# Performance work log

Measured on AMD Instinct MI355X. Metric: run time of the kernel, lower is better.

The kernel has to match this reference:

```python
import jax, jax.numpy as jnp
import numpy as np

B = 16          # graphs per batch
NPER = 1024     # nodes per graph (max_nodes for to_dense_batch)
N = B * NPER    # total nodes
D = 128         # hidden_dim
H = 8           # nhead
E = 524288      # total edges (avg degree 32)
DFF = 512       # dim_feedforward
LN_EPS = 1e-5


def setup_inputs() -> dict:
    key = jax.random.key(0)
    ks = jax.random.split(key, 26)
    w = lambda k, shape, s=0.05: (jax.random.normal(k, shape, jnp.float32) * s)
    h = jax.random.normal(ks[0], (N, D), jnp.float32)
    edge_index = jax.random.randint(ks[1], (2, E), 0, N, jnp.int32)
    edge_attr = jax.random.normal(ks[2], (E, D), jnp.float32)
    # nodes are in a random 'original' order; sort_idx sorts them by graph id
    sort_idx = jax.random.permutation(ks[3], N).astype(jnp.int32)
    unsort_idx = jnp.argsort(sort_idx).astype(jnp.int32)
    sorted_batch = jnp.repeat(jnp.arange(B, dtype=jnp.int32), NPER)
    batch = jnp.zeros((N,), jnp.int32).at[sort_idx].set(sorted_batch)
    return {
        "h": h, "edge_attr": edge_attr,
        # GINEConv: edge linear + 2-layer gin MLP
        "edge_w": w(ks[4], (D, D)), "edge_b": w(ks[5], (D,)),
        "gin_w1": w(ks[6], (D, D)), "gin_b1": w(ks[7], (D,)),
        "gin_w2": w(ks[8], (D, D)), "gin_b2": w(ks[9], (D,)),
        # MultiheadAttention packed qkv + out proj
        "in_proj_w": w(ks[10], (3 * D, D)), "in_proj_b": w(ks[11], (3 * D,)),
        "out_w": w(ks[12], (D, D)), "out_b": w(ks[13], (D,)),
        # FFN
        "ffn_w1": w(ks[14], (DFF, D)), "ffn_b1": w(ks[15], (DFF,)),
        "ffn_w2": w(ks[16], (D, DFF)), "ffn_b2": w(ks[17], (D,)),
        # LayerNorms
        "ln1_w": jnp.ones((D,)), "ln1_b": jnp.zeros((D,)),
        "ln2_w": jnp.ones((D,)), "ln2_b": jnp.zeros((D,)),
        "ln3_w": jnp.ones((D,)), "ln3_b": jnp.zeros((D,)),
        "edge_index": edge_index, "batch": batch,
        "sort_idx": sort_idx, "unsort_idx": unsort_idx,
    }


def _layer_norm(x, w, b):
    mu = x.mean(-1, keepdims=True)
    var = ((x - mu) ** 2).mean(-1, keepdims=True)
    return (x - mu) * jax.lax.rsqrt(var + LN_EPS) * w + b


def reference(h, edge_attr, edge_w, edge_b, gin_w1, gin_b1, gin_w2, gin_b2,
              in_proj_w, in_proj_b, out_w, out_b,
              ffn_w1, ffn_b1, ffn_w2, ffn_b2,
              ln1_w, ln1_b, ln2_w, ln2_b, ln3_w, ln3_b,
              edge_index, batch, sort_idx, unsort_idx):
    residual = h
    # ---- local branch: GINEConv (eps=0) -----------------------------------
    src, dst = edge_index[0], edge_index[1]
    e = edge_attr @ edge_w.T + edge_b                      # [E, D]
    msg = jax.nn.relu(h[src] + e)                          # gather + fuse
    agg = jax.ops.segment_sum(msg, dst, num_segments=N)    # scatter-add
    x = h + agg                                            # (1+eps)*x_i + aggr
    h_local = jax.nn.relu(x @ gin_w1.T + gin_b1) @ gin_w2.T + gin_b2
    # ---- global branch: sort -> dense batch -> MHA -> unsort --------------
    hs = h[sort_idx]
    bs = batch[sort_idx]
    counts = jax.ops.segment_sum(jnp.ones((N,), jnp.int32), bs, num_segments=B)
    ptr = jnp.concatenate([jnp.zeros((1,), jnp.int32),
                           jnp.cumsum(counts)[:-1].astype(jnp.int32)])
    pos = jnp.arange(N, dtype=jnp.int32) - ptr[bs]         # slot within graph
    dense = jnp.zeros((B, NPER, D), h.dtype).at[bs, pos].set(hs)
    mask = jnp.zeros((B, NPER), bool).at[bs, pos].set(True)
    qkv = dense @ in_proj_w.T + in_proj_b                  # [B, NPER, 3D]
    q, k, v = jnp.split(qkv, 3, axis=-1)
    hd = D // H
    q = q.reshape(B, NPER, H, hd)
    k = k.reshape(B, NPER, H, hd)
    v = v.reshape(B, NPER, H, hd)
    scores = jnp.einsum('bqhd,bkhd->bhqk', q, k) / np.float32(np.sqrt(hd))
    scores = jnp.where(mask[:, None, None, :], scores, jnp.float32(-1e9))
    attn = jax.nn.softmax(scores, axis=-1)
    ao = jnp.einsum('bhqk,bkhd->bqhd', attn, v).reshape(B, NPER, D)
    ao = ao @ out_w.T + out_b
    h_attn = ao[bs, pos][unsort_idx]                       # dense->flat->unsort
    # ---- residual + norms + FFN -------------------------------------------
    h1 = _layer_norm(residual + h_local, ln1_w, ln1_b)
    h2 = _layer_norm(h1 + h_attn, ln2_w, ln2_b)
    ffn = jax.nn.gelu(h2 @ ffn_w1.T + ffn_b1, approximate=False) @ ffn_w2.T + ffn_b2
    return _layer_norm(h2 + ffn, ln3_w, ln3_b)
```

## Files before the change

kernel.cpp:

```cpp
#include <hip/hip_runtime.h>
#include <cmath>

typedef __attribute__((ext_vector_type(4))) float  f32x4;
typedef __attribute__((ext_vector_type(16))) float f32x16;
typedef __attribute__((ext_vector_type(2))) float  f32x2;
typedef __attribute__((ext_vector_type(8))) short  s16x8;
typedef __attribute__((ext_vector_type(4))) short  s16x4;
typedef __attribute__((ext_vector_type(2))) short  s16x2;
typedef __attribute__((ext_vector_type(4))) int    i32x4;

#define DEV __device__ __forceinline__

DEV float bf2f(short s) {
    unsigned int u = ((unsigned int)(unsigned short)s) << 16;
    return __builtin_bit_cast(float, u);
}
DEV short f2bs(float f) {
    unsigned int x = __builtin_bit_cast(unsigned int, f);
    x += 0x7fffu + ((x >> 16) & 1u);
    return (short)(x >> 16);
}
DEV s16x8 ld8(const void* p, size_t off, int m) {
    s16x8 r;
    if (m) {
        const float* f = (const float*)p + off;
        f32x4 a = *(const f32x4*)f, b = *(const f32x4*)(f + 4);
#pragma unroll
        for (int j = 0; j < 4; ++j) { r[j] = f2bs(a[j]); r[4 + j] = f2bs(b[j]); }
    } else {
        r = *(const s16x8*)((const short*)p + off);
    }
    return r;
}
DEV float ldf(const void* p, size_t off, int m) {
    return m ? ((const float*)p)[off] : bf2f(((const short*)p)[off]);
}

__global__ void probe_kernel(const unsigned* __restrict__ w1, int* __restrict__ flag)
{
    if (threadIdx.x == 0 && blockIdx.x == 0)
        flag[0] = (w1[0] == 0x3F800000u) ? 1 : 0;
}

__global__ __launch_bounds__(256, 2)
void edge_kernel(const void* __restrict__ EA, const void* __restrict__ EW,
                 const void* __restrict__ EB, const void* __restrict__ H,
                 const int* __restrict__ esrc, const int* __restrict__ edst,
                 float* __restrict__ agg, const int* __restrict__ modep)
{
    const int m = *modep;
    __shared__ short Ws[128][136];
    int tid = threadIdx.x;
#pragma unroll
    for (int i = 0; i < 8; ++i) {
        int id = i * 256 + tid;
        int r = id >> 4, c = (id & 15) << 3;
        *(s16x8*)&Ws[r][c] = ld8(EW, (size_t)r * 128 + c, m);
    }
    __syncthreads();

    int wave = tid >> 6, lane = tid & 63;
    int lq = lane & 15, quad = lane >> 4;
    int eb = blockIdx.x * 64 + wave * 16;

    s16x8 af[4];
    const size_t abase = (size_t)(eb + lq) * 128 + quad * 8;
#pragma unroll
    for (int kb = 0; kb < 4; ++kb)
        af[kb] = ld8(EA, abase + kb * 32, m);

    i32x4 sv = *(const i32x4*)&esrc[eb + quad * 4];
    i32x4 dv = *(const i32x4*)&edst[eb + quad * 4];

    f32x4 acc[8] = {};
#pragma unroll
    for (int kb = 0; kb < 4; ++kb) {
#pragma unroll
        for (int nt = 0; nt < 8; ++nt) {
            s16x8 bfr = *(const s16x8*)&Ws[nt * 16 + lq][kb * 32 + quad * 8];
            acc[nt] = __builtin_amdgcn_mfma_f32_16x16x32_bf16(af[kb], bfr, acc[nt], 0, 0, 0);
        }
    }
#pragma unroll
    for (int nt = 0; nt < 8; ++nt) {
        int col = nt * 16 + lq;
        float bias = ldf(EB, col, m);
#pragma unroll
        for (int r = 0; r < 4; ++r) {
            float v = acc[nt][r] + bias + ldf(H, (size_t)sv[r] * 128 + col, m);
            v = fmaxf(v, 0.f);
            atomicAdd(&agg[(size_t)dv[r] * 128 + col], v);
        }
    }
}

__global__ void xadd_kernel(const void* __restrict__ H, const float* __restrict__ agg,
                            short* __restrict__ X, const int* __restrict__ modep)
{
    const int m = *modep;
    int i = (blockIdx.x * 256 + threadIdx.x) * 4;
    float hv[4];
    if (m) { f32x4 t = *(const f32x4*)((const float*)H + i);
#pragma unroll
             for (int j = 0; j < 4; ++j) hv[j] = t[j]; }
    else   { s16x4 t = *(const s16x4*)((const short*)H + i);
#pragma unroll
             for (int j = 0; j < 4; ++j) hv[j] = bf2f(t[j]); }
    f32x4 av = *(const f32x4*)&agg[i];
    s16x4 o;
#pragma unroll
    for (int j = 0; j < 4; ++j) o[j] = f2bs(hv[j] + av[j]);
    *(s16x4*)&X[i] = o;
}

template<int KTOT, int ACT, bool GATHER, bool XIN>
__global__ __launch_bounds__(256, 2)
void gemm_bt(const void* __restrict__ X, const int* __restrict__ ridx,
             const void* __restrict__ W, const void* __restrict__ B,
             short* __restrict__ Y, int N, const int* __restrict__ modep)
{
    const int m = *modep;
    const int xm = XIN ? m : 0;
    __shared__ short As[64][136];
    __shared__ short Wsh[64][136];
    int tid = threadIdx.x;
    int wave = tid >> 6, lane = tid & 63;
    int lq = lane & 15, quad = lane >> 4;
    int mbase = blockIdx.x * 64, nbase = blockIdx.y * 64;

    f32x4 acc[4] = {};
    for (int kc = 0; kc < KTOT / 128; ++kc) {
#pragma unroll
        for (int i = 0; i < 4; ++i) {
            int id = i * 256 + tid;
            int r = id >> 4, c = (id & 15) << 3;
            int srow = GATHER ? ridx[mbase + r] : (mbase + r);
            *(s16x8*)&As[r][c]  = ld8(X, (size_t)srow * KTOT + kc * 128 + c, xm);
            *(s16x8*)&Wsh[r][c] = ld8(W, (size_t)(nbase + r) * KTOT + kc * 128 + c, m);
        }
        __syncthreads();
        s16x8 af[4];
#pragma unroll
        for (int kb = 0; kb < 4; ++kb)
            af[kb] = *(const s16x8*)&As[wave * 16 + lq][kb * 32 + quad * 8];
#pragma unroll
        for (int kb = 0; kb < 4; ++kb) {
#pragma unroll
            for (int nt = 0; nt < 4; ++nt) {
                s16x8 bfr = *(const s16x8*)&Wsh[nt * 16 + lq][kb * 32 + quad * 8];
                acc[nt] = __builtin_amdgcn_mfma_f32_16x16x32_bf16(af[kb], bfr, acc[nt], 0, 0, 0);
            }
        }
        __syncthreads();
    }
#pragma unroll
    for (int nt = 0; nt < 4; ++nt) {
        int col = nbase + nt * 16 + lq;
        float bias = ldf(B, col, m);
#pragma unroll
        for (int r = 0; r < 4; ++r) {
            int row = mbase + wave * 16 + quad * 4 + r;
            float v = acc[nt][r] + bias;
            if (ACT == 1) v = fmaxf(v, 0.f);
            if (ACT == 2) v = 0.5f * v * (1.f + erff(v * 0.70710678118f));
            Y[(size_t)row * N + col] = f2bs(v);
        }
    }
}

__global__ __launch_bounds__(256, 2)
void attn_kernel(const short* __restrict__ QKV, short* __restrict__ AO)
{
    __shared__ __align__(16) short Ks[2048][8];
    __shared__ __align__(16) short Vt[16][1032];
    int bid = blockIdx.x;
    int qc = bid & 3, bh = bid >> 2;
    int b = bh >> 3, hh = bh & 7;
    int t = threadIdx.x;
    const short* base = QKV + (size_t)b * 1024 * 384 + hh * 16;

#pragma unroll
    for (int i = 0; i < 8; ++i) {
        int idx = i * 256 + t;
        int c = idx >> 10, kv = idx & 1023;
        const short* r = base + (size_t)kv * 384;
        *(s16x8*)&Ks[c * 1024 + kv][0] = *(const s16x8*)&r[128 + c * 8];
        s16x8 v = *(const s16x8*)&r[256 + c * 8];
#pragma unroll
        for (int j = 0; j < 8; ++j) Vt[c * 8 + j][kv] = v[j];
    }
    __syncthreads();

    int wave = t >> 6, lane = t & 63;
    int ln = lane & 31, hi = lane >> 5;

    for (int t2 = 0; t2 < 2; ++t2) {
        int qrow = qc * 256 + t2 * 128 + wave * 32 + ln;
        s16x8 qf = *(const s16x8*)(base + (size_t)qrow * 384 + hi * 8);
        f32x16 oacc = {};
        f32x16 zacc = {};
        float den = 0.f;
        for (int kv0 = 0; kv0 < 1024; kv0 += 32) {
            s16x8 kf = *(const s16x8*)&Ks[hi * 1024 + kv0 + ln][0];
            f32x16 st = __builtin_amdgcn_mfma_f32_32x32x16_bf16(kf, qf, zacc, 0, 0, 0);
            float e[16];
#pragma unroll
            for (int r2 = 0; r2 < 16; ++r2) {
                e[r2] = __expf(fminf(st[r2] * 0.25f, 30.f));
                den += e[r2];
            }
            unsigned pw[8];
#pragma unroll
            for (int r2 = 0; r2 < 8; ++r2)
                pw[r2] = (unsigned)(unsigned short)f2bs(e[2 * r2])
                       | ((unsigned)(unsigned short)f2bs(e[2 * r2 + 1]) << 16);
            auto sA = __builtin_amdgcn_permlane32_swap((int)pw[0], (int)pw[2], false, false);
            auto sB = __builtin_amdgcn_permlane32_swap((int)pw[1], (int)pw[3], false, false);
            auto sC = __builtin_amdgcn_permlane32_swap((int)pw[4], (int)pw[6], false, false);
            auto sD = __builtin_amdgcn_permlane32_swap((int)pw[5], (int)pw[7], false, false);
            i32x4 f1 = { (int)sA[0], (int)sB[0], (int)sA[1], (int)sB[1] };
            i32x4 f2 = { (int)sC[0], (int)sD[0], (int)sC[1], (int)sD[1] };
            s16x8 vf1 = *(const s16x8*)&Vt[ln & 15][kv0 + hi * 8];
            s16x8 vf2 = *(const s16x8*)&Vt[ln & 15][kv0 + 16 + hi * 8];
            oacc = __builtin_amdgcn_mfma_f32_32x32x16_bf16(vf1, __builtin_bit_cast(s16x8, f1), oacc, 0, 0, 0);
            oacc = __builtin_amdgcn_mfma_f32_32x32x16_bf16(vf2, __builtin_bit_cast(s16x8, f2), oacc, 0, 0, 0);
        }
        den += __shfl_xor(den, 32);
        float inv = 1.f / den;
        short* orow = AO + (size_t)(b * 1024 + qrow) * 128 + hh * 16;
        s16x4 oA, oB;
#pragma unroll
        for (int r2 = 0; r2 < 4; ++r2) {
            oA[r2] = f2bs(oacc[r2] * inv);
            oB[r2] = f2bs(oacc[4 + r2] * inv);
        }
        *(s16x4*)&orow[hi * 4]     = oA;
        *(s16x4*)&orow[8 + hi * 4] = oB;
    }
}

template<bool AIN, bool FINAL>
__global__ __launch_bounds__(256)
void ln_kernel(const void* __restrict__ A, const short* __restrict__ Badd,
               const int* __restrict__ gidx,
               const void* __restrict__ w, const void* __restrict__ bb,
               void* __restrict__ outp, const int* __restrict__ modep)
{
    const int m = *modep;
    int wave = threadIdx.x >> 6, lane = threadIdx.x & 63;
    int row = blockIdx.x * 4 + wave;
    int grow = gidx ? gidx[row] : row;
    int c = lane * 2;
    float a0, a1;
    if (AIN && m) {
        f32x2 t = *(const f32x2*)&((const float*)A)[(size_t)row * 128 + c];
        a0 = t[0]; a1 = t[1];
    } else {
        s16x2 t = *(const s16x2*)&((const short*)A)[(size_t)row * 128 + c];
        a0 = bf2f(t[0]); a1 = bf2f(t[1]);
    }
    s16x2 bv = *(const s16x2*)&Badd[(size_t)grow * 128 + c];
    float x0 = a0 + bf2f(bv[0]);
    float x1 = a1 + bf2f(bv[1]);
    float s = x0 + x1;
#pragma unroll
    for (int o = 1; o < 64; o <<= 1) s += __shfl_xor(s, o);
    float mu = s * (1.f / 128.f);
    float d0 = x0 - mu, d1 = x1 - mu;
    float q = d0 * d0 + d1 * d1;
#pragma unroll
    for (int o = 1; o < 64; o <<= 1) q += __shfl_xor(q, o);
    float rs = rsqrtf(q * (1.f / 128.f) + 1e-5f);
    float y0 = d0 * rs * ldf(w, c, m)     + ldf(bb, c, m);
    float y1 = d1 * rs * ldf(w, c + 1, m) + ldf(bb, c + 1, m);
    if (FINAL && m) {
        f32x2 ov = {y0, y1};
        *(f32x2*)&((float*)outp)[(size_t)row * 128 + c] = ov;
    } else {
        s16x2 ov = {f2bs(y0), f2bs(y1)};
        *(s16x2*)&((short*)outp)[(size_t)row * 128 + c] = ov;
    }
}

extern "C" void kernel_launch(void* const* d_in, const int* in_sizes, int n_in,
                              void* d_out, int out_size, void* d_ws, size_t ws_size,
                              hipStream_t stream)
{
    const void* h   = d_in[0];
    const void* ea  = d_in[1];
    const void* edw = d_in[2];
    const void* edb = d_in[3];
    const void* gw1 = d_in[4];
    const void* gb1 = d_in[5];
    const void* gw2 = d_in[6];
    const void* gb2 = d_in[7];
    const void* ipw = d_in[8];
    const void* ipb = d_in[9];
    const void* ow  = d_in[10];
    const void* ob  = d_in[11];
    const void* fw1 = d_in[12];
    const void* fb1 = d_in[13];
    const void* fw2 = d_in[14];
    const void* fb2 = d_in[15];
    const void* l1w = d_in[16];
    const void* l1b = d_in[17];
    const void* l2w = d_in[18];
    const void* l2b = d_in[19];
    const void* l3w = d_in[20];
    const void* l3b = d_in[21];
    const int* ei    = (const int*)d_in[22];
    const int* sidx  = (const int*)d_in[24];
    const int* uidx  = (const int*)d_in[25];

    const int NN = 16384, EE = 524288;
    const size_t MB = 1024 * 1024;
    char* ws = (char*)d_ws;
    float* agg   = (float*)ws;
    short* mid   = (short*)(ws + 8 * MB);
    short* h1    = (short*)(ws + 12 * MB);
    short* qkv   = (short*)ws;
    short* atns  = (short*)(ws + 16 * MB);
    short* ffmid = (short*)ws;
    short* ffout = (short*)(ws + 16 * MB);
    short* h2    = (short*)(ws + 20 * MB);
    int*   flag  = (int*)(ws + 24 * MB);
    short* xbuf  = (short*)d_out;
    short* hloc  = (short*)d_out;
    short* ao    = (short*)d_out;

    probe_kernel<<<1, 64, 0, stream>>>((const unsigned*)l1w, flag);
    hipMemsetAsync(agg, 0, (size_t)NN * 128 * sizeof(float), stream);
    edge_kernel<<<EE / 64, 256, 0, stream>>>(ea, edw, edb, h, ei, ei + EE, agg, flag);
    xadd_kernel<<<NN * 128 / 1024, 256, 0, stream>>>(h, agg, xbuf, flag);
    gemm_bt<128, 1, false, false><<<dim3(NN / 64, 2), 256, 0, stream>>>(xbuf, nullptr, gw1, gb1, mid, 128, flag);
    gemm_bt<128, 0, false, false><<<dim3(NN / 64, 2), 256, 0, stream>>>(mid, nullptr, gw2, gb2, hloc, 128, flag);
    ln_kernel<true, false><<<NN / 4, 256, 0, stream>>>(h, hloc, nullptr, l1w, l1b, h1, flag);
    gemm_bt<128, 0, true, true><<<dim3(NN / 64, 6), 256, 0, stream>>>(h, sidx, ipw, ipb, qkv, 384, flag);
    attn_kernel<<<512, 256, 0, stream>>>(qkv, ao);
    gemm_bt<128, 0, false, false><<<dim3(NN / 64, 2), 256, 0, stream>>>(ao, nullptr, ow, ob, atns, 128, flag);
    ln_kernel<false, false><<<NN / 4, 256, 0, stream>>>(h1, atns, uidx, l2w, l2b, h2, flag);
    gemm_bt<128, 2, false, false><<<dim3(NN / 64, 8), 256, 0, stream>>>(h2, nullptr, fw1, fb1, ffmid, 512, flag);
    gemm_bt<512, 0, false, false><<<dim3(NN / 64, 2), 256, 0, stream>>>(ffmid, nullptr, fw2, fb2, ffout, 128, flag);
    ln_kernel<false, true><<<NN / 4, 256, 0, stream>>>(h2, ffout, nullptr, l3w, l3b, d_out, flag);
}
```

Measured before the change: 757.2 us.

## Sort edges by destination and aggregate runs before atomic adds

Adds a histogram, a single-block scan and a scatter pass that build a CSR-style ordering of edges by destination node. The edge kernel then walks the sorted edges and sums consecutive same-destination contributions in registers before issuing atomics, which cuts the number of global float atomics. The cost is three extra kernels plus one more memset, gathered rather than contiguous reads of edge_attr through sEid, and run-length merging that only spans 16 edges per lane group, which is about half a node's average degree of 32.

```diff
diff --git a/kernel.cpp b/kernel.cpp
--- a/kernel.cpp
+++ b/kernel.cpp
@@ -42,11 +42,52 @@
         flag[0] = (w1[0] == 0x3F800000u) ? 1 : 0;
 }
 
+__global__ void hist_kernel(const int* __restrict__ edst, int* __restrict__ cnt)
+{
+    int e = blockIdx.x * 256 + threadIdx.x;
+    atomicAdd(&cnt[edst[e]], 1);
+}
+
+__global__ __launch_bounds__(1024)
+void scan_kernel(const int* __restrict__ cnt, int* __restrict__ cursor)
+{
+    __shared__ int s[1024];
+    int t = threadIdx.x;
+    int v[16];
+    int sum = 0;
+#pragma unroll
+    for (int j = 0; j < 16; ++j) { v[j] = cnt[t * 16 + j]; sum += v[j]; }
+    s[t] = sum;
+    __syncthreads();
+    for (int off = 1; off < 1024; off <<= 1) {
+        int x = (t >= off) ? s[t - off] : 0;
+        __syncthreads();
+        s[t] += x;
+        __syncthreads();
+    }
+    int running = s[t] - sum;
+#pragma unroll
+    for (int j = 0; j < 16; ++j) { cursor[t * 16 + j] = running; running += v[j]; }
+}
+
+__global__ void scatter_kernel(const int* __restrict__ esrc, const int* __restrict__ edst,
+                               int* __restrict__ cursor, int* __restrict__ sEid,
+                               int* __restrict__ sDst, int* __restrict__ sSrc)
+{
+    int e = blockIdx.x * 256 + threadIdx.x;
+    int d = edst[e];
+    int pos = atomicAdd(&cursor[d], 1);
+    sEid[pos] = e;
+    sDst[pos] = d;
+    sSrc[pos] = esrc[e];
+}
+
 __global__ __launch_bounds__(256, 2)
-void edge_kernel(const void* __restrict__ EA, const void* __restrict__ EW,
-                 const void* __restrict__ EB, const void* __restrict__ H,
-                 const int* __restrict__ esrc, const int* __restrict__ edst,
-                 float* __restrict__ agg, const int* __restrict__ modep)
+void edge_agg_kernel(const void* __restrict__ EA, const void* __restrict__ EW,
+                     const void* __restrict__ EB, const void* __restrict__ H,
+                     const int* __restrict__ sEid, const int* __restrict__ sDst,
+                     const int* __restrict__ sSrc,
+                     float* __restrict__ agg, const int* __restrict__ modep)
 {
     const int m = *modep;
     __shared__ short Ws[128][136];
@@ -61,36 +102,61 @@
 
     int wave = tid >> 6, lane = tid & 63;
     int lq = lane & 15, quad = lane >> 4;
-    int eb = blockIdx.x * 64 + wave * 16;
-
-    s16x8 af[4];
-    const size_t abase = (size_t)(eb + lq) * 128 + quad * 8;
-#pragma unroll
-    for (int kb = 0; kb < 4; ++kb)
-        af[kb] = ld8(EA, abase + kb * 32, m);
-
-    i32x4 sv = *(const i32x4*)&esrc[eb + quad * 4];
-    i32x4 dv = *(const i32x4*)&edst[eb + quad * 4];
-
-    f32x4 acc[8] = {};
-#pragma unroll
-    for (int kb = 0; kb < 4; ++kb) {
-#pragma unroll
-        for (int nt = 0; nt < 8; ++nt) {
-            s16x8 bfr = *(const s16x8*)&Ws[nt * 16 + lq][kb * 32 + quad * 8];
-            acc[nt] = __builtin_amdgcn_mfma_f32_16x16x32_bf16(af[kb], bfr, acc[nt], 0, 0, 0);
-        }
-    }
-#pragma unroll
-    for (int nt = 0; nt < 8; ++nt) {
-        int col = nt * 16 + lq;
-        float bias = ldf(EB, col, m);
+    int ebw = blockIdx.x * 256 + wave * 64;
+
+    float ebias[8];
+#pragma unroll
+    for (int nt = 0; nt < 8; ++nt) ebias[nt] = ldf(EB, nt * 16 + lq, m);
+
+    float run[8] = {};
+    int run_d = -1;
+
+    for (int t = 0; t < 4; ++t) {
+        int arow = ebw + ((lq >> 2) << 4) + t * 4 + (lq & 3);
+        int aeid = sEid[arow];
+        s16x8 af[4];
+        const size_t abase = (size_t)aeid * 128 + quad * 8;
+#pragma unroll
+        for (int kb = 0; kb < 4; ++kb)
+            af[kb] = ld8(EA, abase + kb * 32, m);
+
+        f32x4 acc[8] = {};
+#pragma unroll
+        for (int kb = 0; kb < 4; ++kb) {
+#pragma unroll
+            for (int nt = 0; nt < 8; ++nt) {
+                s16x8 bfr = *(const s16x8*)&Ws[nt * 16 + lq][kb * 32 + quad * 8];
+                acc[nt] = __builtin_amdgcn_mfma_f32_16x16x32_bf16(af[kb], bfr, acc[nt], 0, 0, 0);
+            }
+        }
+
+        int pbase = ebw + quad * 16 + t * 4;
+        i32x4 dv = *(const i32x4*)&sDst[pbase];
+        i32x4 sv = *(const i32x4*)&sSrc[pbase];
 #pragma unroll
         for (int r = 0; r < 4; ++r) {
-            float v = acc[nt][r] + bias + ldf(H, (size_t)sv[r] * 128 + col, m);
-            v = fmaxf(v, 0.f);
-            atomicAdd(&agg[(size_t)dv[r] * 128 + col], v);
-        }
+            int d = dv[r];
+            if (d != run_d) {
+                if (run_d >= 0) {
+#pragma unroll
+                    for (int nt = 0; nt < 8; ++nt)
+                        atomicAdd(&agg[(size_t)run_d * 128 + nt * 16 + lq], run[nt]);
+                }
+                run_d = d;
+#pragma unroll
+                for (int nt = 0; nt < 8; ++nt) run[nt] = 0.f;
+            }
+#pragma unroll
+            for (int nt = 0; nt < 8; ++nt) {
+                float v = acc[nt][r] + ebias[nt] + ldf(H, (size_t)sv[r] * 128 + nt * 16 + lq, m);
+                run[nt] += fmaxf(v, 0.f);
+            }
+        }
+    }
+    if (run_d >= 0) {
+#pragma unroll
+        for (int nt = 0; nt < 8; ++nt)
+            atomicAdd(&agg[(size_t)run_d * 128 + nt * 16 + lq], run[nt]);
     }
 }
 
@@ -324,13 +390,22 @@
     short* ffout = (short*)(ws + 16 * MB);
     short* h2    = (short*)(ws + 20 * MB);
     int*   flag  = (int*)(ws + 24 * MB);
+    int* cnt    = (int*)(ws + 8 * MB);
+    int* cursor = (int*)(ws + 8 * MB + 65536);
+    int* sEid   = (int*)(ws + 9 * MB);
+    int* sDst   = (int*)(ws + 11 * MB);
+    int* sSrc   = (int*)(ws + 13 * MB);
     short* xbuf  = (short*)d_out;
     short* hloc  = (short*)d_out;
     short* ao    = (short*)d_out;
 
     probe_kernel<<<1, 64, 0, stream>>>((const unsigned*)l1w, flag);
     hipMemsetAsync(agg, 0, (size_t)NN * 128 * sizeof(float), stream);
-    edge_kernel<<<EE / 64, 256, 0, stream>>>(ea, edw, edb, h, ei, ei + EE, agg, flag);
+    hipMemsetAsync(cnt, 0, (size_t)NN * sizeof(int), stream);
+    hist_kernel<<<EE / 256, 256, 0, stream>>>(ei + EE, cnt);
+    scan_kernel<<<1, 1024, 0, stream>>>(cnt, cursor);
+    scatter_kernel<<<EE / 256, 256, 0, stream>>>(ei, ei + EE, cursor, sEid, sDst, sSrc);
+    edge_agg_kernel<<<EE / 256, 256, 0, stream>>>(ea, edw, edb, h, sEid, sDst, sSrc, agg, flag);
     xadd_kernel<<<NN * 128 / 1024, 256, 0, stream>>>(h, agg, xbuf, flag);
     gemm_bt<128, 1, false, false><<<dim3(NN / 64, 2), 256, 0, stream>>>(xbuf, nullptr, gw1, gb1, mid, 128, flag);
     gemm_bt<128, 0, false, false><<<dim3(NN / 64, 2), 256, 0, stream>>>(mid, nullptr, gw2, gb2, hloc, 128, flag);
```

Result: faster. 716.8 us (-5.3%).
